# Kernel optimization log

Measured on AMD Instinct MI355X. Metric: run time of the kernel, lower is better.

## Reference

```python
import jax, jax.numpy as jnp
import numpy as np

B, C, F, TP = 16, 64, 128, 100
E = 576
NFEAT, NHID, NOUT = 128, 128, 64
RATIO = 0.9
BN_EPS = 1e-5


def setup_inputs() -> dict:
    key = jax.random.key(0)
    ks = jax.random.split(key, 16)
    s = 0.05
    h = jax.random.normal(ks[0], (B, C, F, TP), jnp.float32)
    edge_index = jax.random.randint(ks[1], (2, E), 0, C, dtype=jnp.int32)
    edge_weight = jax.random.uniform(ks[2], (E,), jnp.float32)
    W1 = jax.random.normal(ks[3], (NFEAT, NHID), jnp.float32) / np.float32(np.sqrt(NFEAT))
    b1 = s * jax.random.normal(ks[4], (NHID,), jnp.float32)
    g1 = 1.0 + s * jax.random.normal(ks[5], (NHID,), jnp.float32)
    be1 = s * jax.random.normal(ks[6], (NHID,), jnp.float32)
    a1 = jnp.full((1,), 0.25, jnp.float32)  # PReLU slope
    Wp = jax.random.normal(ks[7], (NHID, 1), jnp.float32) / np.float32(np.sqrt(NHID))
    bp = s * jax.random.normal(ks[8], (1,), jnp.float32)
    W2 = jax.random.normal(ks[9], (NHID, NOUT), jnp.float32) / np.float32(np.sqrt(NHID))
    b2 = s * jax.random.normal(ks[10], (NOUT,), jnp.float32)
    g2 = 1.0 + s * jax.random.normal(ks[11], (NOUT,), jnp.float32)
    be2 = s * jax.random.normal(ks[12], (NOUT,), jnp.float32)
    a2 = jnp.full((1,), 0.25, jnp.float32)
    return dict(h=h, edge_index=edge_index, edge_weight=edge_weight,
                W1=W1, b1=b1, g1=g1, be1=be1, a1=a1, Wp=Wp, bp=bp,
                W2=W2, b2=b2, g2=g2, be2=be2, a2=a2)


def gcn_conv(x, W, b, row, col, ew, N):
    # PyG GCNConv: add self-loops (weight 1), symmetric normalization, x@W, scatter-add to col.
    si = jnp.arange(N, dtype=row.dtype)
    r = jnp.concatenate([row, si])
    c = jnp.concatenate([col, si])
    w = jnp.concatenate([ew, jnp.ones((N,), x.dtype)])
    deg = jax.ops.segment_sum(w, c, num_segments=N)
    dis = jnp.where(deg > 0, jax.lax.rsqrt(jnp.maximum(deg, 1e-12)), 0.0)
    norm = dis[r] * w * dis[c]
    hlin = x @ W
    out = jax.ops.segment_sum(hlin[r] * norm[:, None], c, num_segments=N)
    return out + b


def batchnorm(x, g, beta):
    m = jnp.mean(x, axis=0)
    v = jnp.mean((x - m) ** 2, axis=0)  # biased var, as in torch BN training
    return (x - m) * jax.lax.rsqrt(v + BN_EPS) * g + beta


def prelu(x, a):
    return jnp.where(x >= 0, x, a * x)


def reference(h, edge_index, edge_weight, W1, b1, g1, be1, a1, Wp, bp, W2, b2, g2, be2, a2):
    Bv, Cv, Fv, Tpv = h.shape
    G = Bv * Tpv                      # num_graphs
    N = G * Cv                        # total nodes
    K = int(np.ceil(RATIO * Cv))      # kept nodes per graph (static)
    x = jnp.transpose(h, (0, 3, 1, 2)).reshape(N, Fv)
    Ev = edge_index.shape[1]
    offs = jnp.repeat(jnp.arange(G, dtype=edge_index.dtype) * Cv, Ev)
    row = jnp.tile(edge_index[0], G) + offs
    col = jnp.tile(edge_index[1], G) + offs
    ew = jnp.tile(edge_weight, G)
    # gc1 -> bn1 -> prelu
    x = prelu(batchnorm(gcn_conv(x, W1, b1, row, col, ew, N), g1, be1), a1)
    # SAGPooling: score GNN (GCNConv, no edge weights), tanh, per-graph top-k
    score = jnp.tanh(gcn_conv(x, Wp, bp, row, col, jnp.ones_like(ew), N)[:, 0])
    topv, topi = jax.lax.top_k(score.reshape(G, Cv), K)
    perm = (topi + (jnp.arange(G, dtype=topi.dtype) * Cv)[:, None]).reshape(-1)
    xk = x[perm] * topv.reshape(-1)[:, None]
    Nk = G * K
    new_id = jnp.zeros((N,), jnp.int32).at[perm].set(jnp.arange(Nk, dtype=jnp.int32))
    kept = jnp.zeros((N,), bool).at[perm].set(True)
    valid = kept[row] & kept[col]
    r2 = new_id[row]
    c2 = new_id[col]
    w2 = jnp.where(valid, ew, 0.0)    # dropped edges: weight 0 == filtered out
    # gc2 -> bn2 -> prelu (dropout is identity in eval)
    x2 = prelu(batchnorm(gcn_conv(xk, W2, b2, r2, c2, w2, Nk), g2, be2), a2)
    # global mean pool: exactly K nodes per graph, contiguous
    z = x2.reshape(G, K, -1).mean(axis=1)
    z_seq = jnp.transpose(z.reshape(Bv, Tpv, -1), (0, 2, 1))
    return x2, z_seq
```

## Files before the change

### kernel.cpp

```cpp
#include <hip/hip_runtime.h>

constexpr int Bc   = 16;
constexpr int Cc   = 64;
constexpr int Fc   = 128;
constexpr int TPc  = 100;
constexpr int Gc   = Bc * TPc;
constexpr int Nc   = Gc * Cc;
constexpr int Ec   = 576;
constexpr int NHID = 128;
constexpr int NOUTc= 64;
constexpr int Kc   = 58;
constexpr int Nkc  = Gc * Kc;

__global__ void k0_prep(const int* __restrict__ ei, const float* __restrict__ ew,
                        float* __restrict__ A1, float* __restrict__ AP,
                        double* bn1S, double* bn1Q, double* bn2S, double* bn2Q) {
    __shared__ float deg1[64], degP[64], dis1[64], disP[64];
    __shared__ float A1L[4096], APL[4096];
    int t = threadIdx.x;
    if (t < 64) { deg1[t] = 1.0f; degP[t] = 1.0f; }
    for (int i = t; i < 4096; i += 256) { A1L[i] = 0.f; APL[i] = 0.f; }
    if (t < 128) { bn1S[t] = 0.0; bn1Q[t] = 0.0; }
    if (t < 64)  { bn2S[t] = 0.0; bn2Q[t] = 0.0; }
    __syncthreads();
    for (int e = t; e < Ec; e += 256) {
        int c = ei[Ec + e];
        atomicAdd(&deg1[c], ew[e]);
        atomicAdd(&degP[c], 1.0f);
    }
    __syncthreads();
    if (t < 64) { dis1[t] = 1.0f / sqrtf(deg1[t]); disP[t] = 1.0f / sqrtf(degP[t]); }
    __syncthreads();
    for (int e = t; e < Ec; e += 256) {
        int r = ei[e], c = ei[Ec + e];
        atomicAdd(&A1L[c * 64 + r], dis1[r] * ew[e] * dis1[c]);
        atomicAdd(&APL[c * 64 + r], disP[r] * disP[c]);
    }
    __syncthreads();
    if (t < 64) {
        A1L[t * 65] += dis1[t] * dis1[t];
        APL[t * 65] += disP[t] * disP[t];
    }
    __syncthreads();
    for (int i = t; i < 4096; i += 256) { A1[i] = A1L[i]; AP[i] = APL[i]; }
}

__global__ __launch_bounds__(256)
void k_trans(const float* __restrict__ h, float* __restrict__ XT) {
    __shared__ float tile[64 * 101];
    int blk = blockIdx.x;
    int b = blk >> 7, f = blk & 127;
    int t = threadIdx.x;
    const float* hb = h + (size_t)b * 819200 + (size_t)f * 100;
    for (int i = t; i < 6400; i += 256) {
        unsigned c = (unsigned)i / 100u;
        unsigned tp = (unsigned)i - c * 100u;
        tile[c * 101 + tp] = hb[(size_t)c * 12800 + tp];
    }
    __syncthreads();
    float* xb = XT + (size_t)b * 100 * 8192 + f * 64;
    for (int j = t; j < 6400; j += 256) {
        int tp = j >> 6, c = j & 63;
        xb[(size_t)tp * 8192 + c] = tile[c * 101 + tp];
    }
}

__global__ __launch_bounds__(256, 4)
void k1_gc1(const float* __restrict__ XT, const float* __restrict__ W1,
            const float* __restrict__ b1, const float* __restrict__ A1,
            float* __restrict__ Y1, double* bn1S, double* bn1Q) {
    __shared__ float Xh[8192];
    int g = blockIdx.x;
    int t = threadIdx.x;
    int tx = t & 31, ty = t >> 5;

    float acc[8][4];
#pragma unroll
    for (int i = 0; i < 8; ++i)
#pragma unroll
        for (int j = 0; j < 4; ++j) acc[i][j] = 0.f;

    for (int kq = 0; kq < 4; ++kq) {
        __syncthreads();
        {
            const float4* xsrc = (const float4*)(XT + (size_t)g * 8192 + kq * 2048);
            float4* xdst = (float4*)Xh;
            xdst[t]       = xsrc[t];
            xdst[256 + t] = xsrc[256 + t];
            const float4* wsrc = (const float4*)(W1 + kq * 4096);
            float4* wdst = (float4*)(Xh + 2048);
#pragma unroll
            for (int it = 0; it < 4; ++it) wdst[it * 256 + t] = wsrc[it * 256 + t];
        }
        __syncthreads();
        for (int kk = 0; kk < 32; ++kk) {
            float4 x0 = *(const float4*)&Xh[kk * 64 + ty * 8];
            float4 x1 = *(const float4*)&Xh[kk * 64 + ty * 8 + 4];
            float4 w  = *(const float4*)&Xh[2048 + kk * 128 + tx * 4];
            float xr[8] = {x0.x, x0.y, x0.z, x0.w, x1.x, x1.y, x1.z, x1.w};
#pragma unroll
            for (int i = 0; i < 8; ++i) {
                acc[i][0] += xr[i] * w.x;
                acc[i][1] += xr[i] * w.y;
                acc[i][2] += xr[i] * w.z;
                acc[i][3] += xr[i] * w.w;
            }
        }
    }
    __syncthreads();
#pragma unroll
    for (int i = 0; i < 8; ++i) {
        float4 v = make_float4(acc[i][0], acc[i][1], acc[i][2], acc[i][3]);
        *(float4*)&Xh[(ty * 8 + i) * 128 + tx * 4] = v;
    }
    __syncthreads();
    float acy[8][4];
    float4 bb = *(const float4*)&b1[tx * 4];
#pragma unroll
    for (int i = 0; i < 8; ++i) { acy[i][0] = bb.x; acy[i][1] = bb.y; acy[i][2] = bb.z; acy[i][3] = bb.w; }
    for (int rr = 0; rr < 16; ++rr) {
        float4 hrow[4];
#pragma unroll
        for (int q = 0; q < 4; ++q) hrow[q] = *(const float4*)&Xh[(rr * 4 + q) * 128 + tx * 4];
#pragma unroll
        for (int i = 0; i < 8; ++i) {
            float4 a4 = *(const float4*)&A1[(ty * 8 + i) * 64 + rr * 4];
            acy[i][0] += a4.x * hrow[0].x + a4.y * hrow[1].x + a4.z * hrow[2].x + a4.w * hrow[3].x;
            acy[i][1] += a4.x * hrow[0].y + a4.y * hrow[1].y + a4.z * hrow[2].y + a4.w * hrow[3].y;
            acy[i][2] += a4.x * hrow[0].z + a4.y * hrow[1].z + a4.z * hrow[2].z + a4.w * hrow[3].z;
            acy[i][3] += a4.x * hrow[0].w + a4.y * hrow[1].w + a4.z * hrow[2].w + a4.w * hrow[3].w;
        }
    }
    float ps[4] = {0, 0, 0, 0}, pq[4] = {0, 0, 0, 0};
    float* Yg = Y1 + (size_t)g * 64 * 128;
#pragma unroll
    for (int i = 0; i < 8; ++i) {
        float4 v = make_float4(acy[i][0], acy[i][1], acy[i][2], acy[i][3]);
        *(float4*)&Yg[(ty * 8 + i) * 128 + tx * 4] = v;
#pragma unroll
        for (int j = 0; j < 4; ++j) { ps[j] += acy[i][j]; pq[j] += acy[i][j] * acy[i][j]; }
    }
    __syncthreads();
    float* redS = Xh;
    float* redQ = Xh + 1024;
#pragma unroll
    for (int j = 0; j < 4; ++j) {
        redS[ty * 128 + tx * 4 + j] = ps[j];
        redQ[ty * 128 + tx * 4 + j] = pq[j];
    }
    __syncthreads();
    if (t < 128) {
        float S = 0.f, Q = 0.f;
        for (int y = 0; y < 8; ++y) { S += redS[y * 128 + t]; Q += redQ[y * 128 + t]; }
        atomicAdd(&bn1S[t], (double)S);
        atomicAdd(&bn1Q[t], (double)Q);
    }
}

__global__ void k_bnfin(const double* __restrict__ S, const double* __restrict__ Q,
                        const float* __restrict__ gam, const float* __restrict__ bet,
                        float* __restrict__ scale, float* __restrict__ shift, double invN) {
    int t = threadIdx.x;
    double m = S[t] * invN;
    double v = Q[t] * invN - m * m;
    double rstd = 1.0 / sqrt(v + 1e-5);
    float sc = (float)((double)gam[t] * rstd);
    scale[t] = sc;
    shift[t] = bet[t] - (float)m * sc;
}

__global__ __launch_bounds__(256, 2)
void k3a_pool(float* __restrict__ Y1, const float* __restrict__ scale1,
              const float* __restrict__ shift1, const float* __restrict__ a1,
              const float* __restrict__ Wp, const float* __restrict__ bp,
              const float* __restrict__ AP, const float* __restrict__ W2) {
    __shared__ float Xs[64 * 132];
    __shared__ float slin[64], psum[256], score[64];
    __shared__ int   rnk[64], ord[64];
    int g = blockIdx.x, t = threadIdx.x;
    int tx = t & 31, ty = t >> 5;
    float alpha1 = a1[0];

    float* slab = Y1 + (size_t)g * 8192;
    {
        const float4* Yg4 = (const float4*)slab;
        float4 sc4 = *(const float4*)&scale1[tx * 4];
        float4 sh4 = *(const float4*)&shift1[tx * 4];
#pragma unroll
        for (int it = 0; it < 8; ++it) {
            int e4 = it * 256 + t;
            int c = e4 >> 5;
            float4 v = Yg4[e4];
            v.x = v.x * sc4.x + sh4.x; v.x = (v.x >= 0.f) ? v.x : alpha1 * v.x;
            v.y = v.y * sc4.y + sh4.y; v.y = (v.y >= 0.f) ? v.y : alpha1 * v.y;
            v.z = v.z * sc4.z + sh4.z; v.z = (v.z >= 0.f) ? v.z : alpha1 * v.z;
            v.w = v.w * sc4.w + sh4.w; v.w = (v.w >= 0.f) ? v.w : alpha1 * v.w;
            *(float4*)&Xs[c * 132 + tx * 4] = v;
        }
    }
    __syncthreads();
    {
        int rr = t >> 2, q4 = t & 3;
        float sp = 0.f;
        for (int m = 0; m < 32; ++m) sp += Xs[rr * 132 + q4 * 32 + m] * Wp[q4 * 32 + m];
        psum[t] = sp;
    }
    __syncthreads();
    if (t < 64) slin[t] = psum[t * 4] + psum[t * 4 + 1] + psum[t * 4 + 2] + psum[t * 4 + 3];
    __syncthreads();
    {
        int n = t >> 2, q = t & 3;
        float acc = 0.f;
#pragma unroll
        for (int m = 0; m < 16; ++m) acc += AP[n * 64 + q * 16 + m] * slin[q * 16 + m];
        psum[t] = acc;
    }
    __syncthreads();
    if (t < 64) score[t] = tanhf(bp[0] + psum[t * 4] + psum[t * 4 + 1] + psum[t * 4 + 2] + psum[t * 4 + 3]);
    __syncthreads();
    {
        int n = t >> 2, q = t & 3;
        float sc = score[n];
        int cnt = 0;
#pragma unroll
        for (int m = 0; m < 16; ++m) {
            int c2 = q * 16 + m;
            float o = score[c2];
            cnt += (o > sc) || (o == sc && c2 < n);
        }
        psum[t] = (float)cnt;
    }
    __syncthreads();
    if (t < 64) {
        int cnt = (int)(psum[t * 4] + psum[t * 4 + 1] + psum[t * 4 + 2] + psum[t * 4 + 3]);
        rnk[t] = cnt;
        if (cnt < Kc) ord[cnt] = t;
        ((int*)(slab + 4096))[t] = cnt;
    }
    __syncthreads();

    {
        int row0 = ty * 8;
        float acc2[8][2];
        int   cidx[8];
        float srow[8];
#pragma unroll
        for (int i = 0; i < 8; ++i) {
            acc2[i][0] = 0.f; acc2[i][1] = 0.f;
            int r = row0 + i;
            if (r < Kc) { cidx[i] = ord[r]; srow[i] = score[cidx[i]]; }
            else        { cidx[i] = 0;      srow[i] = 0.f; }
        }
        for (int k0 = 0; k0 < 128; k0 += 4) {
            float4 xv[8];
#pragma unroll
            for (int i = 0; i < 8; ++i) xv[i] = *(const float4*)&Xs[cidx[i] * 132 + k0];
#pragma unroll
            for (int q = 0; q < 4; ++q) {
                float2 w = *(const float2*)&W2[(k0 + q) * 64 + tx * 2];
#pragma unroll
                for (int i = 0; i < 8; ++i) {
                    float xq = (q == 0) ? xv[i].x : (q == 1) ? xv[i].y : (q == 2) ? xv[i].z : xv[i].w;
                    acc2[i][0] += xq * w.x;
                    acc2[i][1] += xq * w.y;
                }
            }
        }
#pragma unroll
        for (int i = 0; i < 8; ++i) {
            *(float2*)&slab[(row0 + i) * 64 + tx * 2] =
                make_float2(acc2[i][0] * srow[i], acc2[i][1] * srow[i]);
        }
    }
}

__global__ __launch_bounds__(256, 2)
void k3b_gc2(const float* __restrict__ Y1, const int* __restrict__ ei,
             const float* __restrict__ ew, const float* __restrict__ b2,
             float* __restrict__ Y2, double* bn2S, double* bn2Q) {
    __shared__ float H2s[64 * 68];
    __shared__ float A2s[4096];
    __shared__ float dis2[64], deg2[64];
    __shared__ int   rnk[64];
    int g = blockIdx.x, t = threadIdx.x;
    int tx = t & 31, ty = t >> 5;

    const float* slab = Y1 + (size_t)g * 8192;
    {
        const float4* src = (const float4*)slab;
#pragma unroll
        for (int it = 0; it < 4; ++it) {
            int i4 = it * 256 + t;
            int r = i4 >> 4, c4 = i4 & 15;
            *(float4*)&H2s[r * 68 + c4 * 4] = src[i4];
        }
    }
    if (t < 64) rnk[t] = ((const int*)(slab + 4096))[t];
    {
        float4 z = make_float4(0.f, 0.f, 0.f, 0.f);
        float4* A2s4 = (float4*)A2s;
#pragma unroll
        for (int j = 0; j < 4; ++j) A2s4[j * 256 + t] = z;
    }
    if (t < 64) deg2[t] = 1.0f;
    __syncthreads();
    for (int e = t; e < Ec; e += 256) {
        int r = ei[e], c = ei[Ec + e];
        if (rnk[r] < Kc && rnk[c] < Kc) atomicAdd(&deg2[rnk[c]], ew[e]);
    }
    __syncthreads();
    if (t < 64) dis2[t] = 1.0f / sqrtf(deg2[t]);
    __syncthreads();
    for (int e = t; e < Ec; e += 256) {
        int r = ei[e], c = ei[Ec + e];
        int rkr = rnk[r], rkc = rnk[c];
        if (rkr < Kc && rkc < Kc) atomicAdd(&A2s[rkc * 64 + rkr], dis2[rkr] * ew[e] * dis2[rkc]);
    }
    __syncthreads();
    if (t < Kc) A2s[t * 65] += dis2[t] * dis2[t];
    __syncthreads();

    float acy[8][2];
    float2 b2v = *(const float2*)&b2[tx * 2];
#pragma unroll
    for (int i = 0; i < 8; ++i) { acy[i][0] = b2v.x; acy[i][1] = b2v.y; }
    for (int rr = 0; rr < 16; ++rr) {
        float2 h2[4];
#pragma unroll
        for (int q = 0; q < 4; ++q) h2[q] = *(const float2*)&H2s[(rr * 4 + q) * 68 + tx * 2];
#pragma unroll
        for (int i = 0; i < 8; ++i) {
            float4 a4 = *(const float4*)&A2s[(ty * 8 + i) * 64 + rr * 4];
            acy[i][0] += a4.x * h2[0].x + a4.y * h2[1].x + a4.z * h2[2].x + a4.w * h2[3].x;
            acy[i][1] += a4.x * h2[0].y + a4.y * h2[1].y + a4.z * h2[2].y + a4.w * h2[3].y;
        }
    }
    float s0 = 0.f, s1 = 0.f, q0 = 0.f, q1 = 0.f;
    float* Y2g = Y2 + (size_t)g * Kc * 64;
#pragma unroll
    for (int i = 0; i < 8; ++i) {
        int ck = ty * 8 + i;
        if (ck < Kc) {
            float2 v = make_float2(acy[i][0], acy[i][1]);
            *(float2*)&Y2g[ck * 64 + tx * 2] = v;
            s0 += v.x; s1 += v.y; q0 += v.x * v.x; q1 += v.y * v.y;
        }
    }
    __syncthreads();
    float* redS = H2s;
    float* redQ = H2s + 512;
    redS[ty * 64 + tx * 2]     = s0;
    redS[ty * 64 + tx * 2 + 1] = s1;
    redQ[ty * 64 + tx * 2]     = q0;
    redQ[ty * 64 + tx * 2 + 1] = q1;
    __syncthreads();
    if (t < 64) {
        float S = 0.f, Q = 0.f;
        for (int y = 0; y < 8; ++y) { S += redS[y * 64 + t]; Q += redQ[y * 64 + t]; }
        atomicAdd(&bn2S[t], (double)S);
        atomicAdd(&bn2Q[t], (double)Q);
    }
}

__global__ void k5_out(const float* __restrict__ Y2, const float* __restrict__ scale2,
                       const float* __restrict__ shift2, const float* __restrict__ a2v,
                       float* __restrict__ out) {
    __shared__ float red[4 * 64];
    int g = blockIdx.x, t = threadIdx.x;
    float alpha = a2v[0];
    const float* Yg = Y2 + (size_t)g * Kc * 64;
    float* Og = out + (size_t)g * Kc * 64;
    int c = t & 63, rg = t >> 6;
    float part = 0.f;
    for (int rk = rg; rk < Kc; rk += 4) {
        float v = Yg[rk * 64 + c] * scale2[c] + shift2[c];
        v = (v >= 0.f) ? v : alpha * v;
        Og[rk * 64 + c] = v;
        part += v;
    }
    red[rg * 64 + c] = part;
    __syncthreads();
    if (t < 64) {
        float z = (red[t] + red[64 + t] + red[128 + t] + red[192 + t]) / (float)Kc;
        int b = g / TPc, tp = g % TPc;
        out[(size_t)Nkc * 64 + (size_t)b * NOUTc * TPc + t * TPc + tp] = z;
    }
}

extern "C" void kernel_launch(void* const* d_in, const int* in_sizes, int n_in,
                              void* d_out, int out_size, void* d_ws, size_t ws_size,
                              hipStream_t stream) {
    const float* h   = (const float*)d_in[0];
    const int*   ei  = (const int*)  d_in[1];
    const float* ew  = (const float*)d_in[2];
    const float* W1  = (const float*)d_in[3];
    const float* b1  = (const float*)d_in[4];
    const float* g1  = (const float*)d_in[5];
    const float* be1 = (const float*)d_in[6];
    const float* a1  = (const float*)d_in[7];
    const float* Wp  = (const float*)d_in[8];
    const float* bp  = (const float*)d_in[9];
    const float* W2  = (const float*)d_in[10];
    const float* b2  = (const float*)d_in[11];
    const float* g2  = (const float*)d_in[12];
    const float* be2 = (const float*)d_in[13];
    const float* a2  = (const float*)d_in[14];

    char* ws = (char*)d_ws;
    double* bn1S   = (double*)(ws + 0);
    double* bn1Q   = (double*)(ws + 1024);
    double* bn2S   = (double*)(ws + 2048);
    double* bn2Q   = (double*)(ws + 2560);
    float*  scale1 = (float*)(ws + 3072);
    float*  shift1 = (float*)(ws + 3584);
    float*  scale2 = (float*)(ws + 4096);
    float*  shift2 = (float*)(ws + 4352);
    float*  A1     = (float*)(ws + 4608);
    float*  AP     = (float*)(ws + 20992);
    float*  XT     = (float*)(ws + 37376);
    float*  Y1     = XT;
    float*  Y2     = (float*)(ws + 37376 + 52428800);
    float*  out    = (float*)d_out;

    hipLaunchKernelGGL(k0_prep, dim3(1), dim3(256), 0, stream,
                       ei, ew, A1, AP, bn1S, bn1Q, bn2S, bn2Q);
    hipLaunchKernelGGL(k_trans, dim3(2048), dim3(256), 0, stream, h, XT);
    hipLaunchKernelGGL(k1_gc1, dim3(Gc), dim3(256), 0, stream,
                       XT, W1, b1, A1, Y1, bn1S, bn1Q);
    hipLaunchKernelGGL(k_bnfin, dim3(1), dim3(128), 0, stream,
                       bn1S, bn1Q, g1, be1, scale1, shift1, 1.0 / (double)Nc);
    hipLaunchKernelGGL(k3a_pool, dim3(Gc), dim3(256), 0, stream,
                       Y1, scale1, shift1, a1, Wp, bp, AP, W2);
    hipLaunchKernelGGL(k3b_gc2, dim3(Gc), dim3(256), 0, stream,
                       Y1, ei, ew, b2, Y2, bn2S, bn2Q);
    hipLaunchKernelGGL(k_bnfin, dim3(1), dim3(64), 0, stream,
                       bn2S, bn2Q, g2, be2, scale2, shift2, 1.0 / (double)Nkc);
    hipLaunchKernelGGL(k5_out, dim3(Gc), dim3(256), 0, stream,
                       Y2, scale2, shift2, a2, out);
}
```

Measured before the change: 220.5 us.

## Double-buffer gc1 GEMM tiles with async global-to-LDS loads

Replaces the register-staged copy of the XT and W1 k-slices into shared memory in k1_gc1 with direct global_load_lds DMA writes, double-buffered across two LDS slots. The next slice is fetched while the current one is being multiplied, and one barrier per iteration is dropped. This is meant to hide global load latency and save VGPR traffic. In exchange, shared memory grows to 48KB and launch bounds drop to 3 blocks per SM. Correctness depends on the barrier waiting for the async LDS writes to complete.

```diff
diff --git a/kernel.cpp b/kernel.cpp
--- a/kernel.cpp
+++ b/kernel.cpp
@@ -12,6 +12,10 @@
 constexpr int Kc   = 58;
 constexpr int Nkc  = Gc * Kc;
 
+#define GLOAD16(gp, lp) __builtin_amdgcn_global_load_lds( \
+    (const __attribute__((address_space(1))) void*)(gp),  \
+    (__attribute__((address_space(3))) void*)(lp), 16, 0, 0)
+
 __global__ void k0_prep(const int* __restrict__ ei, const float* __restrict__ ew,
                         float* __restrict__ A1, float* __restrict__ AP,
                         double* bn1S, double* bn1Q, double* bn2S, double* bn2Q) {
@@ -65,14 +69,30 @@
     }
 }
 
-__global__ __launch_bounds__(256, 4)
+__global__ __launch_bounds__(256, 3)
 void k1_gc1(const float* __restrict__ XT, const float* __restrict__ W1,
             const float* __restrict__ b1, const float* __restrict__ A1,
             float* __restrict__ Y1, double* bn1S, double* bn1Q) {
-    __shared__ float Xh[8192];
+    __shared__ float S[12288];
     int g = blockIdx.x;
     int t = threadIdx.x;
     int tx = t & 31, ty = t >> 5;
+    int wbase = t & ~63;
+
+    const float4* xsrc = (const float4*)(XT + (size_t)g * 8192);
+    const float4* wsrc = (const float4*)W1;
+
+    auto stage = [&](int qi, int bufsel) {
+        float* buf = S + bufsel * 6144;
+        const float4* xq = xsrc + qi * 512;
+        const float4* wq = wsrc + qi * 1024;
+        GLOAD16(xq + t,       &buf[(size_t)wbase * 4]);
+        GLOAD16(xq + 256 + t, &buf[(size_t)(256 + wbase) * 4]);
+        GLOAD16(wq + t,       &buf[2048 + (size_t)wbase * 4]);
+        GLOAD16(wq + 256 + t, &buf[2048 + (size_t)(256 + wbase) * 4]);
+        GLOAD16(wq + 512 + t, &buf[2048 + (size_t)(512 + wbase) * 4]);
+        GLOAD16(wq + 768 + t, &buf[2048 + (size_t)(768 + wbase) * 4]);
+    };
 
     float acc[8][4];
 #pragma unroll
@@ -80,23 +100,15 @@
 #pragma unroll
         for (int j = 0; j < 4; ++j) acc[i][j] = 0.f;
 
+    stage(0, 0);
+    __syncthreads();
     for (int kq = 0; kq < 4; ++kq) {
-        __syncthreads();
-        {
-            const float4* xsrc = (const float4*)(XT + (size_t)g * 8192 + kq * 2048);
-            float4* xdst = (float4*)Xh;
-            xdst[t]       = xsrc[t];
-            xdst[256 + t] = xsrc[256 + t];
-            const float4* wsrc = (const float4*)(W1 + kq * 4096);
-            float4* wdst = (float4*)(Xh + 2048);
-#pragma unroll
-            for (int it = 0; it < 4; ++it) wdst[it * 256 + t] = wsrc[it * 256 + t];
-        }
-        __syncthreads();
+        if (kq < 3) stage(kq + 1, (kq + 1) & 1);
+        const float* cb = S + (kq & 1) * 6144;
         for (int kk = 0; kk < 32; ++kk) {
-            float4 x0 = *(const float4*)&Xh[kk * 64 + ty * 8];
-            float4 x1 = *(const float4*)&Xh[kk * 64 + ty * 8 + 4];
-            float4 w  = *(const float4*)&Xh[2048 + kk * 128 + tx * 4];
+            float4 x0 = *(const float4*)&cb[kk * 64 + ty * 8];
+            float4 x1 = *(const float4*)&cb[kk * 64 + ty * 8 + 4];
+            float4 w  = *(const float4*)&cb[2048 + kk * 128 + tx * 4];
             float xr[8] = {x0.x, x0.y, x0.z, x0.w, x1.x, x1.y, x1.z, x1.w};
 #pragma unroll
             for (int i = 0; i < 8; ++i) {
@@ -106,12 +118,12 @@
                 acc[i][3] += xr[i] * w.w;
             }
         }
-    }
-    __syncthreads();
+        __syncthreads();
+    }
 #pragma unroll
     for (int i = 0; i < 8; ++i) {
         float4 v = make_float4(acc[i][0], acc[i][1], acc[i][2], acc[i][3]);
-        *(float4*)&Xh[(ty * 8 + i) * 128 + tx * 4] = v;
+        *(float4*)&S[(ty * 8 + i) * 128 + tx * 4] = v;
     }
     __syncthreads();
     float acy[8][4];
@@ -121,7 +133,7 @@
     for (int rr = 0; rr < 16; ++rr) {
         float4 hrow[4];
 #pragma unroll
-        for (int q = 0; q < 4; ++q) hrow[q] = *(const float4*)&Xh[(rr * 4 + q) * 128 + tx * 4];
+        for (int q = 0; q < 4; ++q) hrow[q] = *(const float4*)&S[(rr * 4 + q) * 128 + tx * 4];
 #pragma unroll
         for (int i = 0; i < 8; ++i) {
             float4 a4 = *(const float4*)&A1[(ty * 8 + i) * 64 + rr * 4];
@@ -141,8 +153,8 @@
         for (int j = 0; j < 4; ++j) { ps[j] += acy[i][j]; pq[j] += acy[i][j] * acy[i][j]; }
     }
     __syncthreads();
-    float* redS = Xh;
-    float* redQ = Xh + 1024;
+    float* redS = S;
+    float* redQ = S + 1024;
 #pragma unroll
     for (int j = 0; j < 4; ++j) {
         redS[ty * 128 + tx * 4 + j] = ps[j];
@@ -150,9 +162,9 @@
     }
     __syncthreads();
     if (t < 128) {
-        float S = 0.f, Q = 0.f;
-        for (int y = 0; y < 8; ++y) { S += redS[y * 128 + t]; Q += redQ[y * 128 + t]; }
-        atomicAdd(&bn1S[t], (double)S);
+        float Sv = 0.f, Q = 0.f;
+        for (int y = 0; y < 8; ++y) { Sv += redS[y * 128 + t]; Q += redQ[y * 128 + t]; }
+        atomicAdd(&bn1S[t], (double)Sv);
         atomicAdd(&bn1Q[t], (double)Q);
     }
 }
```

Result: slower. 249.6 us (+13.2%).

## Fold prep into transpose kernel and compute BN finalize per block

Applied to the files above, without the earlier changes.

The single-block adjacency/degree prep kernel becomes an extra block (index 2048) of the transpose kernel. The two one-block BN finalize kernels are removed, and each consumer block now recomputes scale and shift from the double sums into shared memory. This drops three kernel launches and their serialization gaps. In exchange every block repeats a small amount of double-precision math and adds a __syncthreads.

```diff
diff --git a/kernel.cpp b/kernel.cpp
--- a/kernel.cpp
+++ b/kernel.cpp
@@ -12,45 +12,50 @@
 constexpr int Kc   = 58;
 constexpr int Nkc  = Gc * Kc;
 
-__global__ void k0_prep(const int* __restrict__ ei, const float* __restrict__ ew,
-                        float* __restrict__ A1, float* __restrict__ AP,
-                        double* bn1S, double* bn1Q, double* bn2S, double* bn2Q) {
-    __shared__ float deg1[64], degP[64], dis1[64], disP[64];
-    __shared__ float A1L[4096], APL[4096];
+__global__ __launch_bounds__(256)
+void k_trans(const float* __restrict__ h, float* __restrict__ XT,
+             const int* __restrict__ ei, const float* __restrict__ ew,
+             float* __restrict__ A1, float* __restrict__ AP,
+             double* bn1S, double* bn1Q, double* bn2S, double* bn2Q) {
+    __shared__ float S[8448];
     int t = threadIdx.x;
-    if (t < 64) { deg1[t] = 1.0f; degP[t] = 1.0f; }
-    for (int i = t; i < 4096; i += 256) { A1L[i] = 0.f; APL[i] = 0.f; }
-    if (t < 128) { bn1S[t] = 0.0; bn1Q[t] = 0.0; }
-    if (t < 64)  { bn2S[t] = 0.0; bn2Q[t] = 0.0; }
-    __syncthreads();
-    for (int e = t; e < Ec; e += 256) {
-        int c = ei[Ec + e];
-        atomicAdd(&deg1[c], ew[e]);
-        atomicAdd(&degP[c], 1.0f);
-    }
-    __syncthreads();
-    if (t < 64) { dis1[t] = 1.0f / sqrtf(deg1[t]); disP[t] = 1.0f / sqrtf(degP[t]); }
-    __syncthreads();
-    for (int e = t; e < Ec; e += 256) {
-        int r = ei[e], c = ei[Ec + e];
-        atomicAdd(&A1L[c * 64 + r], dis1[r] * ew[e] * dis1[c]);
-        atomicAdd(&APL[c * 64 + r], disP[r] * disP[c]);
-    }
-    __syncthreads();
-    if (t < 64) {
-        A1L[t * 65] += dis1[t] * dis1[t];
-        APL[t * 65] += disP[t] * disP[t];
-    }
-    __syncthreads();
-    for (int i = t; i < 4096; i += 256) { A1[i] = A1L[i]; AP[i] = APL[i]; }
-}
-
-__global__ __launch_bounds__(256)
-void k_trans(const float* __restrict__ h, float* __restrict__ XT) {
-    __shared__ float tile[64 * 101];
+    if (blockIdx.x == 2048) {
+        float* A1L  = S;
+        float* APL  = S + 4096;
+        float* deg1 = S + 8192;
+        float* degP = S + 8256;
+        float* dis1 = S + 8320;
+        float* disP = S + 8384;
+        if (t < 64) { deg1[t] = 1.0f; degP[t] = 1.0f; }
+        for (int i = t; i < 4096; i += 256) { A1L[i] = 0.f; APL[i] = 0.f; }
+        if (t < 128) { bn1S[t] = 0.0; bn1Q[t] = 0.0; }
+        if (t < 64)  { bn2S[t] = 0.0; bn2Q[t] = 0.0; }
+        __syncthreads();
+        for (int e = t; e < Ec; e += 256) {
+            int c = ei[Ec + e];
+            atomicAdd(&deg1[c], ew[e]);
+            atomicAdd(&degP[c], 1.0f);
+        }
+        __syncthreads();
+        if (t < 64) { dis1[t] = 1.0f / sqrtf(deg1[t]); disP[t] = 1.0f / sqrtf(degP[t]); }
+        __syncthreads();
+        for (int e = t; e < Ec; e += 256) {
+            int r = ei[e], c = ei[Ec + e];
+            atomicAdd(&A1L[c * 64 + r], dis1[r] * ew[e] * dis1[c]);
+            atomicAdd(&APL[c * 64 + r], disP[r] * disP[c]);
+        }
+        __syncthreads();
+        if (t < 64) {
+            A1L[t * 65] += dis1[t] * dis1[t];
+            APL[t * 65] += disP[t] * disP[t];
+        }
+        __syncthreads();
+        for (int i = t; i < 4096; i += 256) { A1[i] = A1L[i]; AP[i] = APL[i]; }
+        return;
+    }
+    float* tile = S;
     int blk = blockIdx.x;
     int b = blk >> 7, f = blk & 127;
-    int t = threadIdx.x;
     const float* hb = h + (size_t)b * 819200 + (size_t)f * 100;
     for (int i = t; i < 6400; i += 256) {
         unsigned c = (unsigned)i / 100u;
@@ -150,42 +155,42 @@
     }
     __syncthreads();
     if (t < 128) {
-        float S = 0.f, Q = 0.f;
-        for (int y = 0; y < 8; ++y) { S += redS[y * 128 + t]; Q += redQ[y * 128 + t]; }
-        atomicAdd(&bn1S[t], (double)S);
+        float Sv = 0.f, Q = 0.f;
+        for (int y = 0; y < 8; ++y) { Sv += redS[y * 128 + t]; Q += redQ[y * 128 + t]; }
+        atomicAdd(&bn1S[t], (double)Sv);
         atomicAdd(&bn1Q[t], (double)Q);
     }
 }
 
-__global__ void k_bnfin(const double* __restrict__ S, const double* __restrict__ Q,
-                        const float* __restrict__ gam, const float* __restrict__ bet,
-                        float* __restrict__ scale, float* __restrict__ shift, double invN) {
-    int t = threadIdx.x;
-    double m = S[t] * invN;
-    double v = Q[t] * invN - m * m;
-    double rstd = 1.0 / sqrt(v + 1e-5);
-    float sc = (float)((double)gam[t] * rstd);
-    scale[t] = sc;
-    shift[t] = bet[t] - (float)m * sc;
-}
-
 __global__ __launch_bounds__(256, 2)
-void k3a_pool(float* __restrict__ Y1, const float* __restrict__ scale1,
-              const float* __restrict__ shift1, const float* __restrict__ a1,
+void k3a_pool(float* __restrict__ Y1, const double* __restrict__ bn1S,
+              const double* __restrict__ bn1Q, const float* __restrict__ g1,
+              const float* __restrict__ be1, const float* __restrict__ a1,
               const float* __restrict__ Wp, const float* __restrict__ bp,
               const float* __restrict__ AP, const float* __restrict__ W2) {
     __shared__ float Xs[64 * 132];
     __shared__ float slin[64], psum[256], score[64];
+    __shared__ float scl[128], shf[128];
     __shared__ int   rnk[64], ord[64];
     int g = blockIdx.x, t = threadIdx.x;
     int tx = t & 31, ty = t >> 5;
     float alpha1 = a1[0];
 
+    if (t < 128) {
+        double m = bn1S[t] * (1.0 / (double)Nc);
+        double v = bn1Q[t] * (1.0 / (double)Nc) - m * m;
+        double rstd = 1.0 / sqrt(v + 1e-5);
+        float sc = (float)((double)g1[t] * rstd);
+        scl[t] = sc;
+        shf[t] = be1[t] - (float)m * sc;
+    }
+    __syncthreads();
+
     float* slab = Y1 + (size_t)g * 8192;
     {
         const float4* Yg4 = (const float4*)slab;
-        float4 sc4 = *(const float4*)&scale1[tx * 4];
-        float4 sh4 = *(const float4*)&shift1[tx * 4];
+        float4 sc4 = *(const float4*)&scl[tx * 4];
+        float4 sh4 = *(const float4*)&shf[tx * 4];
 #pragma unroll
         for (int it = 0; it < 8; ++it) {
             int e4 = it * 256 + t;
@@ -362,18 +367,29 @@
     }
 }
 
-__global__ void k5_out(const float* __restrict__ Y2, const float* __restrict__ scale2,
-                       const float* __restrict__ shift2, const float* __restrict__ a2v,
+__global__ void k5_out(const float* __restrict__ Y2, const double* __restrict__ bn2S,
+                       const double* __restrict__ bn2Q, const float* __restrict__ g2,
+                       const float* __restrict__ be2, const float* __restrict__ a2v,
                        float* __restrict__ out) {
     __shared__ float red[4 * 64];
+    __shared__ float scl[64], shf[64];
     int g = blockIdx.x, t = threadIdx.x;
     float alpha = a2v[0];
+    if (t < 64) {
+        double m = bn2S[t] * (1.0 / (double)Nkc);
+        double v = bn2Q[t] * (1.0 / (double)Nkc) - m * m;
+        double rstd = 1.0 / sqrt(v + 1e-5);
+        float sc = (float)((double)g2[t] * rstd);
+        scl[t] = sc;
+        shf[t] = be2[t] - (float)m * sc;
+    }
+    __syncthreads();
     const float* Yg = Y2 + (size_t)g * Kc * 64;
     float* Og = out + (size_t)g * Kc * 64;
     int c = t & 63, rg = t >> 6;
     float part = 0.f;
     for (int rk = rg; rk < Kc; rk += 4) {
-        float v = Yg[rk * 64 + c] * scale2[c] + shift2[c];
+        float v = Yg[rk * 64 + c] * scl[c] + shf[c];
         v = (v >= 0.f) ? v : alpha * v;
         Og[rk * 64 + c] = v;
         part += v;
@@ -411,10 +427,6 @@
     double* bn1Q   = (double*)(ws + 1024);
     double* bn2S   = (double*)(ws + 2048);
     double* bn2Q   = (double*)(ws + 2560);
-    float*  scale1 = (float*)(ws + 3072);
-    float*  shift1 = (float*)(ws + 3584);
-    float*  scale2 = (float*)(ws + 4096);
-    float*  shift2 = (float*)(ws + 4352);
     float*  A1     = (float*)(ws + 4608);
     float*  AP     = (float*)(ws + 20992);
     float*  XT     = (float*)(ws + 37376);
@@ -422,19 +434,14 @@
     float*  Y2     = (float*)(ws + 37376 + 52428800);
     float*  out    = (float*)d_out;
 
-    hipLaunchKernelGGL(k0_prep, dim3(1), dim3(256), 0, stream,
-                       ei, ew, A1, AP, bn1S, bn1Q, bn2S, bn2Q);
-    hipLaunchKernelGGL(k_trans, dim3(2048), dim3(256), 0, stream, h, XT);
+    hipLaunchKernelGGL(k_trans, dim3(2049), dim3(256), 0, stream,
+                       h, XT, ei, ew, A1, AP, bn1S, bn1Q, bn2S, bn2Q);
     hipLaunchKernelGGL(k1_gc1, dim3(Gc), dim3(256), 0, stream,
                        XT, W1, b1, A1, Y1, bn1S, bn1Q);
-    hipLaunchKernelGGL(k_bnfin, dim3(1), dim3(128), 0, stream,
-                       bn1S, bn1Q, g1, be1, scale1, shift1, 1.0 / (double)Nc);
     hipLaunchKernelGGL(k3a_pool, dim3(Gc), dim3(256), 0, stream,
-                       Y1, scale1, shift1, a1, Wp, bp, AP, W2);
+                       Y1, bn1S, bn1Q, g1, be1, a1, Wp, bp, AP, W2);
     hipLaunchKernelGGL(k3b_gc2, dim3(Gc), dim3(256), 0, stream,
                        Y1, ei, ew, b2, Y2, bn2S, bn2Q);
-    hipLaunchKernelGGL(k_bnfin, dim3(1), dim3(64), 0, stream,
-                       bn2S, bn2Q, g2, be2, scale2, shift2, 1.0 / (double)Nkc);
     hipLaunchKernelGGL(k5_out, dim3(Gc), dim3(256), 0, stream,
-                       Y2, scale2, shift2, a2, out);
-}
+                       Y2, bn2S, bn2Q, g2, be2, a2, out);
+}
```

Result: faster. 213.4 us (-3.2%).
